# Kernel optimization log

Hardware: AMD Instinct MI355X
Metric: run time of the kernel (lower is better)

The kernel has to match this reference:

```python
import jax, jax.numpy as jnp
import numpy as np

N_NODES = 100000
N_EDGES = 1600000
D_IN = 128
D_OUT = 128
K_HOPS = 2


def gcn_norm(edge_index, num_nodes):
    # Add self-loops (weight 1), compute symmetric normalization
    # norm_e = deg^{-1/2}[src] * deg^{-1/2}[dst], deg over destination index.
    loop = jnp.arange(num_nodes, dtype=edge_index.dtype)
    src = jnp.concatenate([edge_index[0], loop])
    dst = jnp.concatenate([edge_index[1], loop])
    w = jnp.ones(src.shape[0], dtype=jnp.float32)
    deg = jax.ops.segment_sum(w, dst, num_segments=num_nodes)
    dinv = jnp.where(deg > 0, jax.lax.rsqrt(deg), 0.0)
    norm = dinv[src] * dinv[dst]
    return src, dst, norm


def setup_inputs() -> dict:
    key = jax.random.key(0)
    k1, k2, k3, k4 = jax.random.split(key, 4)
    x = jax.random.normal(k1, (N_NODES, D_IN), dtype=jnp.float32)
    edge_index = jax.random.randint(k2, (2, N_EDGES), 0, N_NODES, dtype=jnp.int64)
    # SGConv linear params (Glorot-ish scale)
    W = jax.random.normal(k3, (D_IN, D_OUT), dtype=jnp.float32) / np.sqrt(D_IN)
    b = jnp.zeros((D_OUT,), dtype=jnp.float32)
    return {"x": x, "edge_index": edge_index, "W": W, "b": b}


def reference(x, edge_index, W, b):
    n = x.shape[0]
    src, dst, norm = gcn_norm(edge_index, n)
    h = x
    for _ in range(K_HOPS):
        # gather source features, scale by edge norm, scatter-add to destinations
        h = jax.ops.segment_sum(h[src] * norm[:, None], dst, num_segments=n)
    return h @ W + b
```

## Files before the change

kernel.cpp:

```cpp
#include <hip/hip_runtime.h>
#include <hip/hip_bf16.h>


#define DFEAT 128
#define ELLW 64

typedef __attribute__((ext_vector_type(8))) short short8;
typedef __attribute__((ext_vector_type(4))) float f32x4;

__device__ __forceinline__ float bf2f(unsigned short u) {
    union { unsigned int i; float f; } t;
    t.i = ((unsigned int)u) << 16;
    return t.f;
}

__device__ __forceinline__ unsigned short f2bf(float f) {
    union { float f; unsigned int i; } t;
    t.f = f;
    unsigned int lsb = (t.i >> 16) & 1u;
    t.i += 0x7fffu + lsb;
    return (unsigned short)(t.i >> 16);
}

__device__ __forceinline__ void accum8(float* acc, uint4 u, float w) {
    acc[0] += bf2f((unsigned short)(u.x & 0xffffu)) * w;
    acc[1] += bf2f((unsigned short)(u.x >> 16)) * w;
    acc[2] += bf2f((unsigned short)(u.y & 0xffffu)) * w;
    acc[3] += bf2f((unsigned short)(u.y >> 16)) * w;
    acc[4] += bf2f((unsigned short)(u.z & 0xffffu)) * w;
    acc[5] += bf2f((unsigned short)(u.z >> 16)) * w;
    acc[6] += bf2f((unsigned short)(u.w & 0xffffu)) * w;
    acc[7] += bf2f((unsigned short)(u.w >> 16)) * w;
}

__global__ void k_detect(const unsigned short* __restrict__ xs,
                         const int* __restrict__ ei, int* __restrict__ flags) {
    __shared__ int s_f32, s_oddnz;
    if (threadIdx.x == 0) { s_f32 = 0; s_oddnz = 0; }
    __syncthreads();
    int bad = 0;
    for (int i = threadIdx.x; i < 16384; i += 256) {
        unsigned int e = (xs[i] >> 7) & 0xFFu;
        if (e >= 0xC0u) bad = 1;
    }
    if (bad) atomicOr(&s_f32, 1);
    int oddnz = 0;
    for (int i = threadIdx.x; i < 4096; i += 256) {
        if (ei[2 * i + 1] != 0) oddnz = 1;
    }
    if (oddnz) atomicOr(&s_oddnz, 1);
    __syncthreads();
    if (threadIdx.x == 0) {
        flags[0] = s_f32;
        flags[1] = s_oddnz ? 0 : 1;
    }
}

__global__ __launch_bounds__(256) void k_fill_ell(const int* __restrict__ ei, int E, int n,
                                                  const int* __restrict__ flags,
                                                  int* __restrict__ cnt,
                                                  int* __restrict__ ell) {
    int r = blockIdx.x & 3;
    int c = blockIdx.x >> 2;
    int nchunks = gridDim.x >> 2;
    int chunk = (E + nchunks - 1) / nchunks;
    int e0 = c * chunk;
    int e1 = min(E, e0 + chunk);
    int i64 = flags[1];
    float inv8n = 8.0f / (float)n;
    for (int e = e0 + (int)threadIdx.x; e < e1; e += 256) {
        int d = i64 ? ei[2 * (E + e)] : ei[E + e];
        int own = min((int)((float)d * inv8n), 7);
        if ((own & 3) != r) continue;
        int s = i64 ? ei[2 * e] : ei[e];
        int pos = atomicAdd(cnt + d, 1);
        if (pos < ELLW) ell[(size_t)d * ELLW + pos] = s;
    }
}

__global__ void k_prepB(const void* __restrict__ Wraw, const int* __restrict__ flags,
                        unsigned short* __restrict__ Bf) {
    int t = blockIdx.x * 256 + threadIdx.x;
    if (t >= 2048) return;
    int lane = t & 63;
    int chunk = (t >> 6) & 3;
    int ntile = t >> 8;
    int ncol = ntile * 16 + (lane & 15);
    int k0 = chunk * 32 + (lane >> 4) * 8;
    int isf = flags[0];
    const float* Wf = (const float*)Wraw;
    const unsigned short* Wb = (const unsigned short*)Wraw;
    unsigned short* o = Bf + (size_t)t * 8;
#pragma unroll
    for (int j = 0; j < 8; j++) {
        int idx = (k0 + j) * DFEAT + ncol;
        o[j] = isf ? f2bf(Wf[idx]) : Wb[idx];
    }
}

__global__ __launch_bounds__(256) void k_gemm0(const void* __restrict__ xraw,
                                               const unsigned short* __restrict__ Bf,
                                               const int* __restrict__ flags,
                                               unsigned short* __restrict__ h0, int n) {
    __shared__ unsigned short thi[16 * 136];
    __shared__ unsigned short tlo[16 * 136];
    int wave = threadIdx.x >> 6;
    int lane = threadIdx.x & 63;
    int g = lane >> 4, c = lane & 15;
    int trow = wave * 4 + g;
    int node = blockIdx.x * 16 + trow;
    int isf = flags[0];

    uint4 ohi = {0, 0, 0, 0}, olo = {0, 0, 0, 0};
    if (node < n) {
        if (isf) {
            const float* xf = (const float*)xraw;
            float4 v0 = *(const float4*)(xf + (size_t)node * DFEAT + c * 8);
            float4 v1 = *(const float4*)(xf + (size_t)node * DFEAT + c * 8 + 4);
            float vv[8] = {v0.x, v0.y, v0.z, v0.w, v1.x, v1.y, v1.z, v1.w};
            unsigned short h[8], l[8];
#pragma unroll
            for (int j = 0; j < 8; j++) {
                h[j] = f2bf(vv[j]);
                l[j] = f2bf(vv[j] - bf2f(h[j]));
            }
            ohi.x = (unsigned int)h[0] | ((unsigned int)h[1] << 16);
            ohi.y = (unsigned int)h[2] | ((unsigned int)h[3] << 16);
            ohi.z = (unsigned int)h[4] | ((unsigned int)h[5] << 16);
            ohi.w = (unsigned int)h[6] | ((unsigned int)h[7] << 16);
            olo.x = (unsigned int)l[0] | ((unsigned int)l[1] << 16);
            olo.y = (unsigned int)l[2] | ((unsigned int)l[3] << 16);
            olo.z = (unsigned int)l[4] | ((unsigned int)l[5] << 16);
            olo.w = (unsigned int)l[6] | ((unsigned int)l[7] << 16);
        } else {
            ohi = *(const uint4*)((const unsigned short*)xraw + (size_t)node * DFEAT + c * 8);
        }
    }
    *(uint4*)(thi + trow * 136 + c * 8) = ohi;
    *(uint4*)(tlo + trow * 136 + c * 8) = olo;
    __syncthreads();

    int m = c, quad = g;
    f32x4 acc2[2];
    acc2[0] = (f32x4){0.f, 0.f, 0.f, 0.f};
    acc2[1] = (f32x4){0.f, 0.f, 0.f, 0.f};
#pragma unroll
    for (int c2 = 0; c2 < 4; c2++) {
        short8 ah = *(const short8*)(thi + m * 136 + c2 * 32 + quad * 8);
        short8 al = *(const short8*)(tlo + m * 136 + c2 * 32 + quad * 8);
#pragma unroll
        for (int t = 0; t < 2; t++) {
            int nt = wave * 2 + t;
            short8 bfr = *(const short8*)(Bf + ((size_t)(nt * 4 + c2) * 64 + lane) * 8);
            acc2[t] = __builtin_amdgcn_mfma_f32_16x16x32_bf16(ah, bfr, acc2[t], 0, 0, 0);
            acc2[t] = __builtin_amdgcn_mfma_f32_16x16x32_bf16(al, bfr, acc2[t], 0, 0, 0);
        }
    }

#pragma unroll
    for (int t = 0; t < 2; t++) {
        int col = (wave * 2 + t) * 16 + m;
#pragma unroll
        for (int r = 0; r < 4; r++) {
            int grow = blockIdx.x * 16 + quad * 4 + r;
            if (grow < n) h0[(size_t)grow * DFEAT + col] = f2bf(acc2[t][r]);
        }
    }
}

__device__ __forceinline__ void hop_accum(const unsigned short* __restrict__ fb,
                                          const int* __restrict__ ell,
                                          const int* __restrict__ cnt,
                                          int node, int lane, float* acc) {
    int g = lane >> 4, c = lane & 15;
    int deg = min(cnt[node], ELLW);
    const int* row = ell + (size_t)node * ELLW;
    float wd = rsqrtf((float)(deg + 1));
#pragma unroll
    for (int j = 0; j < 8; j++) acc[j] = 0.f;

    if (g == 0) {
        uint4 u = *(const uint4*)(fb + (size_t)node * DFEAT + c * 8);
        accum8(acc, u, wd * wd);
    }
    int last = deg - 1;
    for (int base = 0; base < deg; base += 16) {
        int k0 = base + g, k1 = k0 + 4, k2 = k0 + 8, k3 = k0 + 12;
        int s0 = row[min(k0, last)];
        int s1 = row[min(k1, last)];
        int s2 = row[min(k2, last)];
        int s3 = row[min(k3, last)];
        uint4 u0 = *(const uint4*)(fb + (size_t)s0 * DFEAT + c * 8);
        uint4 u1 = *(const uint4*)(fb + (size_t)s1 * DFEAT + c * 8);
        uint4 u2 = *(const uint4*)(fb + (size_t)s2 * DFEAT + c * 8);
        uint4 u3 = *(const uint4*)(fb + (size_t)s3 * DFEAT + c * 8);
        float w0 = (k0 < deg) ? rsqrtf((float)(cnt[s0] + 1)) * wd : 0.f;
        float w1 = (k1 < deg) ? rsqrtf((float)(cnt[s1] + 1)) * wd : 0.f;
        float w2 = (k2 < deg) ? rsqrtf((float)(cnt[s2] + 1)) * wd : 0.f;
        float w3 = (k3 < deg) ? rsqrtf((float)(cnt[s3] + 1)) * wd : 0.f;
        accum8(acc, u0, w0);
        accum8(acc, u1, w1);
        accum8(acc, u2, w2);
        accum8(acc, u3, w3);
    }
#pragma unroll
    for (int j = 0; j < 8; j++) {
        acc[j] += __shfl_xor(acc[j], 16);
        acc[j] += __shfl_xor(acc[j], 32);
    }
}

__global__ __launch_bounds__(256) void k_hop(const unsigned short* __restrict__ src,
                                             const int* __restrict__ ell,
                                             const int* __restrict__ cnt,
                                             unsigned short* __restrict__ outb, int n) {
    int node = blockIdx.x * 4 + (threadIdx.x >> 6);
    if (node >= n) return;
    int lane = threadIdx.x & 63;
    int g = lane >> 4, c = lane & 15;
    float acc[8];
    hop_accum(src, ell, cnt, node, lane, acc);
    if (g == 0) {
        uint4 o;
        o.x = (unsigned int)f2bf(acc[0]) | ((unsigned int)f2bf(acc[1]) << 16);
        o.y = (unsigned int)f2bf(acc[2]) | ((unsigned int)f2bf(acc[3]) << 16);
        o.z = (unsigned int)f2bf(acc[4]) | ((unsigned int)f2bf(acc[5]) << 16);
        o.w = (unsigned int)f2bf(acc[6]) | ((unsigned int)f2bf(acc[7]) << 16);
        *(uint4*)(outb + (size_t)node * DFEAT + c * 8) = o;
    }
}

__global__ __launch_bounds__(256) void k_hop2_out(const unsigned short* __restrict__ src,
                                                  const int* __restrict__ ell,
                                                  const int* __restrict__ cnt,
                                                  const void* __restrict__ braw,
                                                  const int* __restrict__ flags,
                                                  void* __restrict__ outraw, int n) {
    int node = blockIdx.x * 4 + (threadIdx.x >> 6);
    if (node >= n) return;
    int lane = threadIdx.x & 63;
    int g = lane >> 4, c = lane & 15;
    float acc[8];
    hop_accum(src, ell, cnt, node, lane, acc);
    if (g == 0) {
        int isf = flags[0];
        const float* bf32 = (const float*)braw;
        const unsigned short* bb16 = (const unsigned short*)braw;
#pragma unroll
        for (int j = 0; j < 8; j++)
            acc[j] += isf ? bf32[c * 8 + j] : bf2f(bb16[c * 8 + j]);
        if (isf) {
            float* outf = (float*)outraw;
            *(float4*)(outf + (size_t)node * DFEAT + c * 8) =
                (float4){acc[0], acc[1], acc[2], acc[3]};
            *(float4*)(outf + (size_t)node * DFEAT + c * 8 + 4) =
                (float4){acc[4], acc[5], acc[6], acc[7]};
        } else {
            unsigned short* outb = (unsigned short*)outraw;
            uint4 o;
            o.x = (unsigned int)f2bf(acc[0]) | ((unsigned int)f2bf(acc[1]) << 16);
            o.y = (unsigned int)f2bf(acc[2]) | ((unsigned int)f2bf(acc[3]) << 16);
            o.z = (unsigned int)f2bf(acc[4]) | ((unsigned int)f2bf(acc[5]) << 16);
            o.w = (unsigned int)f2bf(acc[6]) | ((unsigned int)f2bf(acc[7]) << 16);
            *(uint4*)(outb + (size_t)node * DFEAT + c * 8) = o;
        }
    }
}

extern "C" void kernel_launch(void* const* d_in, const int* in_sizes, int n_in,
                              void* d_out, int out_size, void* d_ws, size_t ws_size,
                              hipStream_t stream) {
    const void* x = d_in[0];
    const int* ei = (const int*)d_in[1];
    const void* W = d_in[2];
    const void* b = d_in[3];

    const int n = in_sizes[0] / DFEAT;
    const int E = in_sizes[1] / 2;

    int* ell = (int*)d_ws;
    unsigned short* h1 = (unsigned short*)(ell + (size_t)n * ELLW);
    int* cnt = (int*)(h1 + (size_t)n * DFEAT);
    int* flags = cnt + n;
    unsigned short* Bf = (unsigned short*)(flags + 4);
    unsigned short* h0 = (unsigned short*)d_out;

    hipMemsetAsync(cnt, 0, (size_t)n * sizeof(int), stream);

    k_detect<<<1, 256, 0, stream>>>((const unsigned short*)x, ei, flags);

    k_fill_ell<<<4 * 2048, 256, 0, stream>>>(ei, E, n, flags, cnt, ell);

    k_prepB<<<8, 256, 0, stream>>>(W, flags, Bf);

    k_gemm0<<<(n + 15) / 16, 256, 0, stream>>>(x, Bf, flags, h0, n);

    k_hop<<<(n + 3) / 4, 256, 0, stream>>>(h0, ell, cnt, h1, n);

    k_hop2_out<<<(n + 3) / 4, 256, 0, stream>>>(h1, ell, cnt, b, flags, d_out, n);
}
```

Before: 371.5 us.

## Fuse ELL fill with first GEMM and use nontemporal loads/stores

```diff
diff --git a/kernel.cpp b/kernel.cpp
--- a/kernel.cpp
+++ b/kernel.cpp
@@ -4,9 +4,11 @@
 
 #define DFEAT 128
 #define ELLW 64
+#define NCHUNK 2048
 
 typedef __attribute__((ext_vector_type(8))) short short8;
 typedef __attribute__((ext_vector_type(4))) float f32x4;
+typedef __attribute__((ext_vector_type(4))) unsigned int u32x4;
 
 __device__ __forceinline__ float bf2f(unsigned short u) {
     union { unsigned int i; float f; } t;
@@ -53,28 +55,6 @@
     if (threadIdx.x == 0) {
         flags[0] = s_f32;
         flags[1] = s_oddnz ? 0 : 1;
-    }
-}
-
-__global__ __launch_bounds__(256) void k_fill_ell(const int* __restrict__ ei, int E, int n,
-                                                  const int* __restrict__ flags,
-                                                  int* __restrict__ cnt,
-                                                  int* __restrict__ ell) {
-    int r = blockIdx.x & 3;
-    int c = blockIdx.x >> 2;
-    int nchunks = gridDim.x >> 2;
-    int chunk = (E + nchunks - 1) / nchunks;
-    int e0 = c * chunk;
-    int e1 = min(E, e0 + chunk);
-    int i64 = flags[1];
-    float inv8n = 8.0f / (float)n;
-    for (int e = e0 + (int)threadIdx.x; e < e1; e += 256) {
-        int d = i64 ? ei[2 * (E + e)] : ei[E + e];
-        int own = min((int)((float)d * inv8n), 7);
-        if ((own & 3) != r) continue;
-        int s = i64 ? ei[2 * e] : ei[e];
-        int pos = atomicAdd(cnt + d, 1);
-        if (pos < ELLW) ell[(size_t)d * ELLW + pos] = s;
     }
 }
 
@@ -98,12 +78,39 @@
     }
 }
 
-__global__ __launch_bounds__(256) void k_gemm0(const void* __restrict__ xraw,
-                                               const unsigned short* __restrict__ Bf,
-                                               const int* __restrict__ flags,
-                                               unsigned short* __restrict__ h0, int n) {
+__global__ __launch_bounds__(256) void k_fill_gemm0(const int* __restrict__ ei, int E, int n,
+                                                    const int* __restrict__ flags,
+                                                    int* __restrict__ cnt,
+                                                    int* __restrict__ ell,
+                                                    const void* __restrict__ xraw,
+                                                    const unsigned short* __restrict__ Bf,
+                                                    unsigned short* __restrict__ h0) {
     __shared__ unsigned short thi[16 * 136];
     __shared__ unsigned short tlo[16 * 136];
+
+    {
+        int r = blockIdx.x & 7;
+        int c = blockIdx.x >> 3;
+        int chunk = (E + NCHUNK - 1) / NCHUNK;
+        int e0 = c * chunk;
+        int e1 = min(E, e0 + chunk);
+        int i64 = flags[1];
+        float inv8n = 8.0f / (float)n;
+        for (int e = e0 + (int)threadIdx.x; e < e1; e += 256) {
+            int d = i64 ? __builtin_nontemporal_load(ei + 2 * (E + e))
+                        : __builtin_nontemporal_load(ei + E + e);
+            int own = min((int)((float)d * inv8n), 7);
+            if (own != r) continue;
+            int s = i64 ? __builtin_nontemporal_load(ei + 2 * e)
+                        : __builtin_nontemporal_load(ei + e);
+            int pos = atomicAdd(cnt + d, 1);
+            if (pos < ELLW) ell[(size_t)d * ELLW + pos] = s;
+        }
+    }
+
+    int g0blocks = (n + 15) >> 4;
+    if (blockIdx.x >= (unsigned)g0blocks) return;
+
     int wave = threadIdx.x >> 6;
     int lane = threadIdx.x & 63;
     int g = lane >> 4, c = lane & 15;
@@ -115,9 +122,9 @@
     if (node < n) {
         if (isf) {
             const float* xf = (const float*)xraw;
-            float4 v0 = *(const float4*)(xf + (size_t)node * DFEAT + c * 8);
-            float4 v1 = *(const float4*)(xf + (size_t)node * DFEAT + c * 8 + 4);
-            float vv[8] = {v0.x, v0.y, v0.z, v0.w, v1.x, v1.y, v1.z, v1.w};
+            f32x4 v0 = __builtin_nontemporal_load((const f32x4*)(xf + (size_t)node * DFEAT + c * 8));
+            f32x4 v1 = __builtin_nontemporal_load((const f32x4*)(xf + (size_t)node * DFEAT + c * 8 + 4));
+            float vv[8] = {v0[0], v0[1], v0[2], v0[3], v1[0], v1[1], v1[2], v1[3]};
             unsigned short h[8], l[8];
 #pragma unroll
             for (int j = 0; j < 8; j++) {
@@ -133,7 +140,9 @@
             olo.z = (unsigned int)l[4] | ((unsigned int)l[5] << 16);
             olo.w = (unsigned int)l[6] | ((unsigned int)l[7] << 16);
         } else {
-            ohi = *(const uint4*)((const unsigned short*)xraw + (size_t)node * DFEAT + c * 8);
+            u32x4 u = __builtin_nontemporal_load(
+                (const u32x4*)((const unsigned short*)xraw + (size_t)node * DFEAT + c * 8));
+            ohi.x = u[0]; ohi.y = u[1]; ohi.z = u[2]; ohi.w = u[3];
         }
     }
     *(uint4*)(thi + trow * 136 + c * 8) = ohi;
@@ -161,9 +170,10 @@
     for (int t = 0; t < 2; t++) {
         int col = (wave * 2 + t) * 16 + m;
 #pragma unroll
-        for (int r = 0; r < 4; r++) {
-            int grow = blockIdx.x * 16 + quad * 4 + r;
-            if (grow < n) h0[(size_t)grow * DFEAT + col] = f2bf(acc2[t][r]);
+        for (int r2 = 0; r2 < 4; r2++) {
+            int grow = blockIdx.x * 16 + quad * 4 + r2;
+            if (grow < n)
+                __builtin_nontemporal_store(f2bf(acc2[t][r2]), h0 + (size_t)grow * DFEAT + col);
         }
     }
 }
@@ -186,10 +196,10 @@
     int last = deg - 1;
     for (int base = 0; base < deg; base += 16) {
         int k0 = base + g, k1 = k0 + 4, k2 = k0 + 8, k3 = k0 + 12;
-        int s0 = row[min(k0, last)];
-        int s1 = row[min(k1, last)];
-        int s2 = row[min(k2, last)];
-        int s3 = row[min(k3, last)];
+        int s0 = __builtin_nontemporal_load(row + min(k0, last));
+        int s1 = __builtin_nontemporal_load(row + min(k1, last));
+        int s2 = __builtin_nontemporal_load(row + min(k2, last));
+        int s3 = __builtin_nontemporal_load(row + min(k3, last));
         uint4 u0 = *(const uint4*)(fb + (size_t)s0 * DFEAT + c * 8);
         uint4 u1 = *(const uint4*)(fb + (size_t)s1 * DFEAT + c * 8);
         uint4 u2 = *(const uint4*)(fb + (size_t)s2 * DFEAT + c * 8);
@@ -289,11 +299,12 @@
 
     k_detect<<<1, 256, 0, stream>>>((const unsigned short*)x, ei, flags);
 
-    k_fill_ell<<<4 * 2048, 256, 0, stream>>>(ei, E, n, flags, cnt, ell);
-
     k_prepB<<<8, 256, 0, stream>>>(W, flags, Bf);
 
-    k_gemm0<<<(n + 15) / 16, 256, 0, stream>>>(x, Bf, flags, h0, n);
+    int g0blocks = (n + 15) / 16;
+    int grid = 8 * NCHUNK;
+    if (g0blocks > grid) grid = g0blocks;
+    k_fill_gemm0<<<grid, 256, 0, stream>>>(ei, E, n, flags, cnt, ell, x, Bf, h0);
 
     k_hop<<<(n + 3) / 4, 256, 0, stream>>>(h0, ell, cnt, h1, n);
 
```

Measured after the change: 382.7 us. 1.03x slower.
